# Kernel optimization log

Hardware: AMD Instinct MI355X
Metric: run time of the kernel (lower is better)

The kernel has to match this reference:

```python
import jax, jax.numpy as jnp
import numpy as np

B, S, HID, NH = 2, 2048, 2048, 16
HD = HID // NH          # head_size = 128
ROPE_THETA = 10000.0
SCALING = HD ** -0.5


def setup_inputs() -> dict:
    key = jax.random.key(0)
    ks = jax.random.split(key, 8)
    std = 1.0 / np.sqrt(HID)
    inp = {
        "hidden_states": jax.random.normal(ks[0], (B, S, HID), jnp.float32),
        "positions": jnp.broadcast_to(jnp.arange(S, dtype=jnp.int32), (B, S)),
        "wq": jax.random.normal(ks[1], (HID, HID), jnp.float32) * std,
        "bq": jax.random.normal(ks[2], (HID,), jnp.float32) * 0.02,
        "wk": jax.random.normal(ks[3], (HID, HID), jnp.float32) * std,
        "bk": jax.random.normal(ks[4], (HID,), jnp.float32) * 0.02,
        "wv": jax.random.normal(ks[5], (HID, HID), jnp.float32) * std,
        "bv": jax.random.normal(ks[6], (HID,), jnp.float32) * 0.02,
        "wc": jax.random.normal(ks[7], (HID, HID), jnp.float32) * std,
    }
    return inp


def _rope_neox(x, positions):
    # x: [B, S, NH, HD]; positions: [B, S] int
    half = HD // 2
    inv_freq = 1.0 / (ROPE_THETA ** (jnp.arange(half, dtype=jnp.float32) * (2.0 / HD)))
    freqs = positions.astype(jnp.float32)[..., None] * inv_freq      # [B,S,half]
    cos = jnp.cos(freqs)[:, :, None, :]                               # [B,S,1,half]
    sin = jnp.sin(freqs)[:, :, None, :]
    x1, x2 = x[..., :half], x[..., half:]
    return jnp.concatenate([x1 * cos - x2 * sin, x2 * cos + x1 * sin], axis=-1)


def reference(hidden_states, positions, wq, bq, wk, bk, wv, bv, wc):
    # fused QKV projections
    q = hidden_states @ wq + bq
    k = hidden_states @ wk + bk
    v = hidden_states @ wv + bv
    q = q.reshape(B, S, NH, HD)
    k = k.reshape(B, S, NH, HD)
    v = v.reshape(B, S, NH, HD)
    # neox-style rotary embedding over full head dim
    q = _rope_neox(q, positions)
    k = _rope_neox(k, positions)
    # causal self-attention (prefill path of RadixAttention)
    scores = jnp.einsum("bqhd,bkhd->bhqk", q, k) * SCALING
    causal = jnp.tril(jnp.ones((S, S), dtype=bool))
    scores = jnp.where(causal, scores, jnp.finfo(scores.dtype).min)
    probs = jax.nn.softmax(scores, axis=-1)
    attn = jnp.einsum("bhqk,bkhd->bqhd", probs, v).reshape(B, S, HID)
    # output projection (no bias)
    return attn @ wc
```

## Files before the change

kernel.cpp:

```cpp
#include <hip/hip_runtime.h>
#include <stdint.h>

constexpr int Bsz = 2;
constexpr int Ssz = 2048;
constexpr int Hid = 2048;
constexpr int NHd = 16;
constexpr int Hd  = 128;
constexpr int Mrows = Bsz * Ssz;
constexpr float kScale = 0.08838834764831845f;

typedef __bf16 bf16;
typedef __bf16 bf16x8 __attribute__((ext_vector_type(8)));
typedef __bf16 bf16x4 __attribute__((ext_vector_type(4)));
typedef float  f32x4  __attribute__((ext_vector_type(4)));
typedef float  f32x16 __attribute__((ext_vector_type(16)));

__device__ __forceinline__ void gload_lds16(const bf16* g, bf16* l) {
  __builtin_amdgcn_global_load_lds((const __attribute__((address_space(1))) void*)g,
                                   (__attribute__((address_space(3))) void*)l, 16, 0, 0);
}

__device__ __forceinline__ uint32_t pkbf(bf16 a, bf16 b) {
  union { bf16 hh[2]; uint32_t u; } x;
  x.hh[0] = a; x.hh[1] = b;
  return x.u;
}
__device__ __forceinline__ uint32_t pkff(float a, float b) {
  return pkbf((bf16)a, (bf16)b);
}

__global__ void k_cvt(const float* __restrict__ in, bf16* __restrict__ out, int n4) {
  int i = blockIdx.x * blockDim.x + threadIdx.x;
  if (i >= n4) return;
  float4 v = ((const float4*)in)[i];
  bf16x4 o = { (bf16)v.x, (bf16)v.y, (bf16)v.z, (bf16)v.w };
  ((bf16x4*)out)[i] = o;
}

__global__ void k_wtrans(const float* __restrict__ w0, const float* __restrict__ w1,
                         const float* __restrict__ w2, const float* __restrict__ w3,
                         bf16* __restrict__ out) {
  __shared__ float tile[32][33];
  int z = blockIdx.z;
  const float* w = (z == 0) ? w0 : (z == 1) ? w1 : (z == 2) ? w2 : w3;
  bf16* o = out + (size_t)z * Hid * Hid;
  int n0 = blockIdx.x * 32, k0 = blockIdx.y * 32;
  int tx = threadIdx.x, ty = threadIdx.y;
#pragma unroll
  for (int i = 0; i < 4; i++)
    tile[ty + i * 8][tx] = w[(size_t)(k0 + ty + i * 8) * Hid + n0 + tx];
  __syncthreads();
#pragma unroll
  for (int i = 0; i < 4; i++)
    o[(size_t)(n0 + ty + i * 8) * Hid + k0 + tx] = (bf16)tile[tx][ty + i * 8];
}

__device__ __forceinline__ bf16x8 rdfrag(const bf16* t, int row, int kslot) {
  return *(const bf16x8*)((const char*)t + row * 128 + (((kslot ^ (row & 7)) & 7) << 4));
}

template <int NB>
__device__ __forceinline__ void stageN(const bf16* g, bf16* l, int w, int lane) {
  const int rsub = lane >> 3;
  const int slot = (lane & 7) ^ rsub;
#pragma unroll
  for (int j = 0; j < NB; ++j) {
    const int blk = w * NB + j;
    gload_lds16(g + (size_t)(blk * 8 + rsub) * Hid + slot * 8, l + blk * 512);
  }
}

#define PH_SYNC()                                      \
  __builtin_amdgcn_s_barrier();                        \
  asm volatile("s_waitcnt lgkmcnt(0)" ::: "memory");   \
  __builtin_amdgcn_sched_barrier(0);

template <int MODE>
__global__ __launch_bounds__(512, 2) void k_gemm(const bf16* __restrict__ A,
                                                 const bf16* __restrict__ Bt,
                                                 const float* __restrict__ biasq,
                                                 const float* __restrict__ biask,
                                                 const float* __restrict__ biasv,
                                                 bf16* __restrict__ Qo, bf16* __restrict__ Ko,
                                                 bf16* __restrict__ Vo, float* __restrict__ Fo) {
  constexpr int KK = Hid;
  constexpr int NT = KK / 64;
  __shared__ bf16 smA[2][256 * 64];
  __shared__ bf16 smB[2][128 * 64];
  const int nwg = gridDim.x * gridDim.y;
  int flat = blockIdx.y * gridDim.x + blockIdx.x;
  flat = (flat & 7) * (nwg >> 3) + (flat >> 3);
  const int m0 = (flat / gridDim.x) * 256;
  const int n0 = (flat % gridDim.x) * 128;
  const int tid = threadIdx.x, lane = tid & 63, w = tid >> 6;
  const int wm = w >> 1, wn = w & 1;
  const int frow = lane & 15, a4 = lane >> 4;
  const bf16* Ag = A + (size_t)m0 * KK;
  const bf16* Bg = Bt + (size_t)n0 * KK;
  f32x4 acc[4][4] = {};
  stageN<4>(Ag, smA[0], w, lane);
  stageN<2>(Bg, smB[0], w, lane);
  __syncthreads();
#pragma unroll 2
  for (int kt = 0; kt < NT; ++kt) {
    const int cur = kt & 1;
    const bf16* At = smA[cur];
    const bf16* Btl = smB[cur];
    bf16* As2 = smA[cur ^ 1];
    bf16* Bs2 = smB[cur ^ 1];
    const int kn = (kt + 1 < NT ? kt + 1 : kt) * 64;
    bf16x8 af[2][2], bfr[4][2];
#pragma unroll
    for (int mi = 0; mi < 2; ++mi)
#pragma unroll
      for (int kk = 0; kk < 2; ++kk)
        af[mi][kk] = rdfrag(At, wm * 64 + mi * 16 + frow, kk * 4 + a4);
#pragma unroll
    for (int ni = 0; ni < 4; ++ni)
#pragma unroll
      for (int kk = 0; kk < 2; ++kk)
        bfr[ni][kk] = rdfrag(Btl, wn * 64 + ni * 16 + frow, kk * 4 + a4);
    stageN<4>(Ag + kn, As2, w, lane);
    PH_SYNC();
    __builtin_amdgcn_s_setprio(1);
#pragma unroll
    for (int mi = 0; mi < 2; ++mi)
#pragma unroll
      for (int ni = 0; ni < 4; ++ni)
#pragma unroll
        for (int kk = 0; kk < 2; ++kk)
          acc[mi][ni] = __builtin_amdgcn_mfma_f32_16x16x32_bf16(
              af[mi][kk], bfr[ni][kk], acc[mi][ni], 0, 0, 0);
    __builtin_amdgcn_s_setprio(0);
    __builtin_amdgcn_s_barrier();
#pragma unroll
    for (int mi = 0; mi < 2; ++mi)
#pragma unroll
      for (int kk = 0; kk < 2; ++kk)
        af[mi][kk] = rdfrag(At, wm * 64 + (2 + mi) * 16 + frow, kk * 4 + a4);
    stageN<2>(Bg + kn, Bs2, w, lane);
    PH_SYNC();
    __builtin_amdgcn_s_setprio(1);
#pragma unroll
    for (int mi = 0; mi < 2; ++mi)
#pragma unroll
      for (int ni = 0; ni < 4; ++ni)
#pragma unroll
        for (int kk = 0; kk < 2; ++kk)
          acc[2 + mi][ni] = __builtin_amdgcn_mfma_f32_16x16x32_bf16(
              af[mi][kk], bfr[ni][kk], acc[2 + mi][ni], 0, 0, 0);
    __builtin_amdgcn_s_setprio(0);
    asm volatile("s_waitcnt vmcnt(0)" ::: "memory");
    __builtin_amdgcn_s_barrier();
  }
  if (MODE == 0) {
    const int z = n0 >> 11;
    const float* bias = (z == 0) ? biasq : (z == 1) ? biask : biasv;
    bf16* o = (z == 0) ? Qo : (z == 1) ? Ko : Vo;
    const float oscale = (z == 1) ? (float)(0.08838834764831845 * 1.4426950408889634) : 1.0f;
#pragma unroll
    for (int ni = 0; ni < 4; ++ni) {
      const int col = n0 + wn * 64 + ni * 16 + frow;
      const float bb_ = bias[col & 2047];
      const int h = (col >> 7) & 15, hd = col & (Hd - 1);
#pragma unroll
      for (int mi = 0; mi < 4; ++mi) {
#pragma unroll
        for (int r = 0; r < 4; ++r) {
          const int row = m0 + wm * 64 + mi * 16 + a4 * 4 + r;
          const int bb = row >> 11, ss = row & (Ssz - 1);
          o[(((size_t)bb * NHd + h) * Ssz + ss) * Hd + hd] = (bf16)((acc[mi][ni][r] + bb_) * oscale);
        }
      }
    }
  } else {
#pragma unroll
    for (int mi = 0; mi < 4; ++mi)
#pragma unroll
      for (int ni = 0; ni < 4; ++ni) {
        const int col = n0 + wn * 64 + ni * 16 + frow;
#pragma unroll
        for (int r = 0; r < 4; ++r) {
          const int row = m0 + wm * 64 + mi * 16 + a4 * 4 + r;
          Fo[(size_t)row * Hid + col] = acc[mi][ni][r];
        }
      }
  }
}

__global__ void k_rope(bf16* __restrict__ Q, bf16* __restrict__ Kk, const int* __restrict__ pos) {
  const int idx = blockIdx.x * 256 + threadIdx.x;
  const int i = idx & 63;
  const int s = (idx >> 6) & (Ssz - 1);
  const int bh = idx >> 17;
  const int b = bh >> 4;
  const float p = (float)pos[b * Ssz + s];
  const float f = p * exp2f(-(float)i * 0.20762050593046014f);
  float sn, cs;
  sincosf(f, &sn, &cs);
  const size_t base = ((size_t)bh * Ssz + s) * Hd;
  float x1 = (float)Q[base + i], x2 = (float)Q[base + i + 64];
  Q[base + i]      = (bf16)(x1 * cs - x2 * sn);
  Q[base + i + 64] = (bf16)(x2 * cs + x1 * sn);
  x1 = (float)Kk[base + i]; x2 = (float)Kk[base + i + 64];
  Kk[base + i]      = (bf16)(x1 * cs - x2 * sn);
  Kk[base + i + 64] = (bf16)(x2 * cs + x1 * sn);
}

__global__ __launch_bounds__(256, 2) void k_attn(const bf16* __restrict__ Qg,
                                                 const bf16* __restrict__ Kg,
                                                 const bf16* __restrict__ Vg,
                                                 bf16* __restrict__ AO) {
  const int bh = blockIdx.y;
  int qc = blockIdx.x;
  if (bh & 1) qc = 15 - qc;
  const int tid = threadIdx.x, lane = tid & 63, w = tid >> 6;
  const int l31 = lane & 31, h = lane >> 5;
  __shared__ bf16 Ks[64 * 128];
  __shared__ bf16 Vt[128 * 72];
  const size_t hbase = (size_t)bh * Ssz * Hd;
  const int q0 = qc * 128 + w * 32;
  bf16x8 qf[8];
  {
    const bf16* qp = Qg + hbase + (size_t)(q0 + l31) * Hd + h * 8;
#pragma unroll
    for (int c = 0; c < 8; c++) qf[c] = *(const bf16x8*)(qp + c * 16);
  }
  float m = -1e30f, lsum = 0.f;
  f32x16 o[4] = {};
  const int NT = 2 * (qc + 1);
  for (int t = 0; t < NT; ++t) {
    const int kv0 = t * 64;
    __syncthreads();
    {
      const bf16* Kt = Kg + hbase + (size_t)kv0 * Hd;
#pragma unroll
      for (int i = 0; i < 4; i++) {
        const int db  = (w * 4 + i) * 1024 + (lane << 4);
        const int row = db >> 8;
        const int cb  = (db & 255) ^ ((row & 7) << 4);
        gload_lds16(Kt + row * Hd + (cb >> 1), Ks + (w * 4 + i) * 512);
      }
    }
    {
      const int r4  = (tid >> 4) << 2;
      const int hd0 = (tid & 15) << 3;
      bf16x8 vv[4];
#pragma unroll
      for (int p = 0; p < 4; p++)
        vv[p] = *(const bf16x8*)(Vg + hbase + (size_t)(kv0 + r4 + p) * Hd + hd0);
#pragma unroll
      for (int j = 0; j < 8; j++) {
        uint2 wv;
        wv.x = pkbf(vv[0][j], vv[1][j]);
        wv.y = pkbf(vv[2][j], vv[3][j]);
        const int hd = hd0 + j;
        const int cb = (r4 * 2) ^ (((hd >> 3) & 7) << 4);
        *(uint2*)((char*)Vt + hd * 144 + cb) = wv;
      }
    }
    __syncthreads();
    if (kv0 <= q0 + 31) {
      f32x16 s0 = {}, s1 = {};
#pragma unroll
      for (int c = 0; c < 8; c++) {
        const int cb = (c * 32 + h * 16) ^ ((l31 & 7) << 4);
        bf16x8 k0 = *(const bf16x8*)((const char*)Ks + l31 * 256 + cb);
        bf16x8 k1 = *(const bf16x8*)((const char*)Ks + (32 + l31) * 256 + cb);
        s0 = __builtin_amdgcn_mfma_f32_32x32x16_bf16(k0, qf[c], s0, 0, 0, 0);
        s1 = __builtin_amdgcn_mfma_f32_32x32x16_bf16(k1, qf[c], s1, 0, 0, 0);
      }
      if (kv0 + 63 > q0) {
        const int qg = q0 + l31;
        const int kb = kv0 + 4 * h;
#pragma unroll
        for (int r = 0; r < 16; r++) {
          const int cr = (r & 3) + 8 * (r >> 2);
          if (kb + cr > qg)      s0[r] = -1e30f;
          if (kb + 32 + cr > qg) s1[r] = -1e30f;
        }
      }
      float tm = s0[0];
#pragma unroll
      for (int r = 1; r < 16; r++) tm = fmaxf(tm, s0[r]);
#pragma unroll
      for (int r = 0; r < 16; r++) tm = fmaxf(tm, s1[r]);
      tm = fmaxf(tm, __shfl_xor(tm, 32));
      if (!__all(tm - m <= 8.0f)) {
        const float mn = fmaxf(m, tm);
        const float rs = exp2f(m - mn);
        m = mn; lsum *= rs;
#pragma unroll
        for (int ct = 0; ct < 4; ct++)
#pragma unroll
          for (int r = 0; r < 16; r++) o[ct][r] *= rs;
      }
      float ps = 0.f;
#pragma unroll
      for (int r = 0; r < 16; r++) { s0[r] = exp2f(s0[r] - m); ps += s0[r]; }
#pragma unroll
      for (int r = 0; r < 16; r++) { s1[r] = exp2f(s1[r] - m); ps += s1[r]; }
      ps += __shfl_xor(ps, 32);
      lsum += ps;
      uint32_t gw[8][2];
#pragma unroll
      for (int g = 0; g < 4; g++) {
        gw[g][0]     = pkff(s0[4 * g], s0[4 * g + 1]);
        gw[g][1]     = pkff(s0[4 * g + 2], s0[4 * g + 3]);
        gw[4 + g][0] = pkff(s1[4 * g], s1[4 * g + 1]);
        gw[4 + g][1] = pkff(s1[4 * g + 2], s1[4 * g + 3]);
      }
#pragma unroll
      for (int kc = 0; kc < 4; kc++) {
        const uint32_t a0 = gw[2 * kc][0], a1 = gw[2 * kc][1];
        const uint32_t b0 = gw[2 * kc + 1][0], b1 = gw[2 * kc + 1][1];
        const uint32_t sd0 = h ? a0 : b0, sd1 = h ? a1 : b1;
        const uint32_t r0 = (uint32_t)__shfl_xor((int)sd0, 32);
        const uint32_t r1 = (uint32_t)__shfl_xor((int)sd1, 32);
        union { uint32_t u[4]; bf16x8 v; } pa;
        pa.u[0] = h ? r0 : a0; pa.u[1] = h ? r1 : a1;
        pa.u[2] = h ? b0 : r0; pa.u[3] = h ? b1 : r1;
#pragma unroll
        for (int ct = 0; ct < 4; ct++) {
          const int row = ct * 32 + l31;
          const int cb = (kc * 32 + h * 16) ^ (((row >> 3) & 7) << 4);
          bf16x8 vf = *(const bf16x8*)((const char*)Vt + row * 144 + cb);
          o[ct] = __builtin_amdgcn_mfma_f32_32x32x16_bf16(pa.v, vf, o[ct], 0, 0, 0);
        }
      }
    }
  }
  const float linv = 1.0f / lsum;
  float li[16];
#pragma unroll
  for (int r = 0; r < 16; r++)
    li[r] = __shfl(linv, (r & 3) + 8 * (r >> 2) + 4 * h);
  const int b = bh >> 4, hh = bh & 15;
#pragma unroll
  for (int ct = 0; ct < 4; ct++) {
#pragma unroll
    for (int r = 0; r < 16; r++) {
      const int qrow = q0 + (r & 3) + 8 * (r >> 2) + 4 * h;
      AO[((size_t)b * Ssz + qrow) * Hid + hh * Hd + ct * 32 + l31] = (bf16)(o[ct][r] * li[r]);
    }
  }
}

extern "C" void kernel_launch(void* const* d_in, const int* in_sizes, int n_in,
                              void* d_out, int out_size, void* d_ws, size_t ws_size,
                              hipStream_t stream) {
  (void)in_sizes; (void)n_in; (void)out_size; (void)ws_size;
  const float* hidden   = (const float*)d_in[0];
  const int*   positions= (const int*)d_in[1];
  const float* wq = (const float*)d_in[2];
  const float* bq = (const float*)d_in[3];
  const float* wk = (const float*)d_in[4];
  const float* bk = (const float*)d_in[5];
  const float* wv = (const float*)d_in[6];
  const float* bv = (const float*)d_in[7];
  const float* wc = (const float*)d_in[8];
  float* out = (float*)d_out;

  char* ws = (char*)d_ws;
  bf16* WT  = (bf16*)ws;
  bf16* Hbf = (bf16*)(ws + (size_t)4 * Hid * Hid * 2);
  bf16* Qb  = (bf16*)(ws + (size_t)4 * Hid * Hid * 2 + (size_t)Mrows * Hid * 2);
  bf16* Kb  = Qb + (size_t)Mrows * Hid;
  bf16* Vb  = Kb + (size_t)Mrows * Hid;

  k_cvt<<<dim3(Mrows * Hid / 4 / 256), dim3(256), 0, stream>>>(hidden, Hbf, Mrows * Hid / 4);
  k_wtrans<<<dim3(Hid / 32, Hid / 32, 4), dim3(32, 8), 0, stream>>>(wq, wk, wv, wc, WT);
  k_gemm<0><<<dim3(48, 16), dim3(512), 0, stream>>>(
      Hbf, WT, bq, bk, bv, Qb, Kb, Vb, nullptr);
  k_rope<<<dim3(Bsz * NHd * Ssz * 64 / 256), dim3(256), 0, stream>>>(Qb, Kb, positions);
  k_attn<<<dim3(16, Bsz * NHd), dim3(256), 0, stream>>>(Qb, Kb, Vb, Hbf );
  k_gemm<1><<<dim3(16, 16), dim3(512), 0, stream>>>(
      Hbf, WT + (size_t)3 * Hid * Hid, nullptr, nullptr, nullptr,
      nullptr, nullptr, nullptr, out);
}
```

Before: 301.2 us.

## Triple-buffer GEMM loads, chunked tile swizzle, and double-buffer attention K/V

The GEMM moves from double to triple buffering of its LDS tiles and prefetches two k-steps ahead with partial vmcnt waits. Its block remapping now walks chunked tiles (CHM x CHN per XCD chunk) to improve L2 reuse. The attention kernel double-buffers K and V in LDS and prefetches the next tile's K/V while the current one is computed. The larger LDS footprint lowers GEMM occupancy to one block per CU (launch bounds 512,1), and the new waitcnt counts must exactly match the number of outstanding loads.

```diff
diff --git a/kernel.cpp b/kernel.cpp
--- a/kernel.cpp
+++ b/kernel.cpp
@@ -7,7 +7,6 @@
 constexpr int NHd = 16;
 constexpr int Hd  = 128;
 constexpr int Mrows = Bsz * Ssz;
-constexpr float kScale = 0.08838834764831845f;
 
 typedef __bf16 bf16;
 typedef __bf16 bf16x8 __attribute__((ext_vector_type(8)));
@@ -75,8 +74,8 @@
   asm volatile("s_waitcnt lgkmcnt(0)" ::: "memory");   \
   __builtin_amdgcn_sched_barrier(0);
 
-template <int MODE>
-__global__ __launch_bounds__(512, 2) void k_gemm(const bf16* __restrict__ A,
+template <int MODE, int CHM, int CHN>
+__global__ __launch_bounds__(512, 1) void k_gemm(const bf16* __restrict__ A,
                                                  const bf16* __restrict__ Bt,
                                                  const float* __restrict__ biasq,
                                                  const float* __restrict__ biask,
@@ -85,13 +84,15 @@
                                                  bf16* __restrict__ Vo, float* __restrict__ Fo) {
   constexpr int KK = Hid;
   constexpr int NT = KK / 64;
-  __shared__ bf16 smA[2][256 * 64];
-  __shared__ bf16 smB[2][128 * 64];
-  const int nwg = gridDim.x * gridDim.y;
-  int flat = blockIdx.y * gridDim.x + blockIdx.x;
-  flat = (flat & 7) * (nwg >> 3) + (flat >> 3);
-  const int m0 = (flat / gridDim.x) * 256;
-  const int n0 = (flat % gridDim.x) * 128;
+  __shared__ bf16 smA[3][256 * 64];
+  __shared__ bf16 smB[3][128 * 64];
+  const int hw = blockIdx.y * gridDim.x + blockIdx.x;
+  const int chunk = hw & 7, within = hw >> 3;
+  const int chunk_rows = gridDim.y / CHM;
+  const int cr = chunk % chunk_rows, cc = chunk / chunk_rows;
+  const int mt = cr * CHM + within % CHM;
+  const int nt = cc * CHN + within / CHM;
+  const int m0 = mt * 256, n0 = nt * 128;
   const int tid = threadIdx.x, lane = tid & 63, w = tid >> 6;
   const int wm = w >> 1, wn = w & 1;
   const int frow = lane & 15, a4 = lane >> 4;
@@ -100,15 +101,16 @@
   f32x4 acc[4][4] = {};
   stageN<4>(Ag, smA[0], w, lane);
   stageN<2>(Bg, smB[0], w, lane);
-  __syncthreads();
-#pragma unroll 2
+  stageN<4>(Ag + 64, smA[1], w, lane);
+  stageN<2>(Bg + 64, smB[1], w, lane);
+  asm volatile("s_waitcnt vmcnt(6)" ::: "memory");
+  __builtin_amdgcn_s_barrier();
   for (int kt = 0; kt < NT; ++kt) {
-    const int cur = kt & 1;
-    const bf16* At = smA[cur];
-    const bf16* Btl = smB[cur];
-    bf16* As2 = smA[cur ^ 1];
-    bf16* Bs2 = smB[cur ^ 1];
-    const int kn = (kt + 1 < NT ? kt + 1 : kt) * 64;
+    const bf16* At  = smA[kt % 3];
+    const bf16* Btl = smB[kt % 3];
+    bf16* As2 = smA[(kt + 2) % 3];
+    bf16* Bs2 = smB[(kt + 2) % 3];
+    const int kn2 = (kt + 2 < NT ? kt + 2 : kt) * 64;
     bf16x8 af[2][2], bfr[4][2];
 #pragma unroll
     for (int mi = 0; mi < 2; ++mi)
@@ -120,7 +122,7 @@
 #pragma unroll
       for (int kk = 0; kk < 2; ++kk)
         bfr[ni][kk] = rdfrag(Btl, wn * 64 + ni * 16 + frow, kk * 4 + a4);
-    stageN<4>(Ag + kn, As2, w, lane);
+    stageN<4>(Ag + kn2, As2, w, lane);
     PH_SYNC();
     __builtin_amdgcn_s_setprio(1);
 #pragma unroll
@@ -138,7 +140,7 @@
 #pragma unroll
       for (int kk = 0; kk < 2; ++kk)
         af[mi][kk] = rdfrag(At, wm * 64 + (2 + mi) * 16 + frow, kk * 4 + a4);
-    stageN<2>(Bg + kn, Bs2, w, lane);
+    stageN<2>(Bg + kn2, Bs2, w, lane);
     PH_SYNC();
     __builtin_amdgcn_s_setprio(1);
 #pragma unroll
@@ -150,7 +152,8 @@
           acc[2 + mi][ni] = __builtin_amdgcn_mfma_f32_16x16x32_bf16(
               af[mi][kk], bfr[ni][kk], acc[2 + mi][ni], 0, 0, 0);
     __builtin_amdgcn_s_setprio(0);
-    asm volatile("s_waitcnt vmcnt(0)" ::: "memory");
+    asm volatile("s_waitcnt vmcnt(6)" ::: "memory");
+    __builtin_amdgcn_sched_barrier(0);
     __builtin_amdgcn_s_barrier();
   }
   if (MODE == 0) {
@@ -216,8 +219,8 @@
   if (bh & 1) qc = 15 - qc;
   const int tid = threadIdx.x, lane = tid & 63, w = tid >> 6;
   const int l31 = lane & 31, h = lane >> 5;
-  __shared__ bf16 Ks[64 * 128];
-  __shared__ bf16 Vt[128 * 72];
+  __shared__ bf16 Ks[2][64 * 128];
+  __shared__ bf16 Vt[2][128 * 72];
   const size_t hbase = (size_t)bh * Ssz * Hd;
   const int q0 = qc * 128 + w * 32;
   bf16x8 qf[8];
@@ -229,44 +232,58 @@
   float m = -1e30f, lsum = 0.f;
   f32x16 o[4] = {};
   const int NT = 2 * (qc + 1);
+  const int r4  = (tid >> 4) << 2;
+  const int hd0 = (tid & 15) << 3;
+  bf16x8 vv[4];
+#pragma unroll
+  for (int p = 0; p < 4; p++)
+    vv[p] = *(const bf16x8*)(Vg + hbase + (size_t)(r4 + p) * Hd + hd0);
+  __builtin_amdgcn_sched_barrier(0);
+#pragma unroll
+  for (int i = 0; i < 4; i++) {
+    const int db  = (w * 4 + i) * 1024 + (lane << 4);
+    const int row = db >> 8;
+    const int cb  = (db & 255) ^ ((row & 7) << 4);
+    gload_lds16(Kg + hbase + row * Hd + (cb >> 1), Ks[0] + (w * 4 + i) * 512);
+  }
   for (int t = 0; t < NT; ++t) {
     const int kv0 = t * 64;
-    __syncthreads();
-    {
-      const bf16* Kt = Kg + hbase + (size_t)kv0 * Hd;
-#pragma unroll
-      for (int i = 0; i < 4; i++) {
-        const int db  = (w * 4 + i) * 1024 + (lane << 4);
-        const int row = db >> 8;
-        const int cb  = (db & 255) ^ ((row & 7) << 4);
-        gload_lds16(Kt + row * Hd + (cb >> 1), Ks + (w * 4 + i) * 512);
-      }
-    }
-    {
-      const int r4  = (tid >> 4) << 2;
-      const int hd0 = (tid & 15) << 3;
-      bf16x8 vv[4];
-#pragma unroll
-      for (int p = 0; p < 4; p++)
-        vv[p] = *(const bf16x8*)(Vg + hbase + (size_t)(kv0 + r4 + p) * Hd + hd0);
-#pragma unroll
-      for (int j = 0; j < 8; j++) {
-        uint2 wv;
-        wv.x = pkbf(vv[0][j], vv[1][j]);
-        wv.y = pkbf(vv[2][j], vv[3][j]);
-        const int hd = hd0 + j;
-        const int cb = (r4 * 2) ^ (((hd >> 3) & 7) << 4);
-        *(uint2*)((char*)Vt + hd * 144 + cb) = wv;
-      }
-    }
-    __syncthreads();
+    const int cur = t & 1;
+    asm volatile("s_waitcnt vmcnt(4)" ::: "memory");
+#pragma unroll
+    for (int j = 0; j < 8; j++) {
+      uint2 wv;
+      wv.x = pkbf(vv[0][j], vv[1][j]);
+      wv.y = pkbf(vv[2][j], vv[3][j]);
+      const int hd = hd0 + j;
+      const int cb = (r4 * 2) ^ (((hd >> 3) & 7) << 4);
+      *(uint2*)((char*)(Vt[cur]) + hd * 144 + cb) = wv;
+    }
+    const int tn = (t + 1 < NT) ? t + 1 : t;
+    const size_t nb = (size_t)tn * 64;
+#pragma unroll
+    for (int p = 0; p < 4; p++)
+      vv[p] = *(const bf16x8*)(Vg + hbase + (nb + r4 + p) * Hd + hd0);
+    __builtin_amdgcn_sched_barrier(0);
+#pragma unroll
+    for (int i = 0; i < 4; i++) {
+      const int db  = (w * 4 + i) * 1024 + (lane << 4);
+      const int row = db >> 8;
+      const int cb  = (db & 255) ^ ((row & 7) << 4);
+      gload_lds16(Kg + hbase + (nb + row) * Hd + (cb >> 1), Ks[cur ^ 1] + (w * 4 + i) * 512);
+    }
+    asm volatile("s_waitcnt vmcnt(8) lgkmcnt(0)" ::: "memory");
+    __builtin_amdgcn_sched_barrier(0);
+    __builtin_amdgcn_s_barrier();
     if (kv0 <= q0 + 31) {
+      const bf16* KsC = Ks[cur];
+      const bf16* VtC = Vt[cur];
       f32x16 s0 = {}, s1 = {};
 #pragma unroll
       for (int c = 0; c < 8; c++) {
         const int cb = (c * 32 + h * 16) ^ ((l31 & 7) << 4);
-        bf16x8 k0 = *(const bf16x8*)((const char*)Ks + l31 * 256 + cb);
-        bf16x8 k1 = *(const bf16x8*)((const char*)Ks + (32 + l31) * 256 + cb);
+        bf16x8 k0 = *(const bf16x8*)((const char*)KsC + l31 * 256 + cb);
+        bf16x8 k1 = *(const bf16x8*)((const char*)KsC + (32 + l31) * 256 + cb);
         s0 = __builtin_amdgcn_mfma_f32_32x32x16_bf16(k0, qf[c], s0, 0, 0, 0);
         s1 = __builtin_amdgcn_mfma_f32_32x32x16_bf16(k1, qf[c], s1, 0, 0, 0);
       }
@@ -324,11 +341,12 @@
         for (int ct = 0; ct < 4; ct++) {
           const int row = ct * 32 + l31;
           const int cb = (kc * 32 + h * 16) ^ (((row >> 3) & 7) << 4);
-          bf16x8 vf = *(const bf16x8*)((const char*)Vt + row * 144 + cb);
+          bf16x8 vf = *(const bf16x8*)((const char*)VtC + row * 144 + cb);
           o[ct] = __builtin_amdgcn_mfma_f32_32x32x16_bf16(pa.v, vf, o[ct], 0, 0, 0);
         }
       }
     }
+    __builtin_amdgcn_s_barrier();
   }
   const float linv = 1.0f / lsum;
   float li[16];
@@ -370,11 +388,11 @@
 
   k_cvt<<<dim3(Mrows * Hid / 4 / 256), dim3(256), 0, stream>>>(hidden, Hbf, Mrows * Hid / 4);
   k_wtrans<<<dim3(Hid / 32, Hid / 32, 4), dim3(32, 8), 0, stream>>>(wq, wk, wv, wc, WT);
-  k_gemm<0><<<dim3(48, 16), dim3(512), 0, stream>>>(
+  k_gemm<0, 8, 12><<<dim3(48, 16), dim3(512), 0, stream>>>(
       Hbf, WT, bq, bk, bv, Qb, Kb, Vb, nullptr);
   k_rope<<<dim3(Bsz * NHd * Ssz * 64 / 256), dim3(256), 0, stream>>>(Qb, Kb, positions);
   k_attn<<<dim3(16, Bsz * NHd), dim3(256), 0, stream>>>(Qb, Kb, Vb, Hbf );
-  k_gemm<1><<<dim3(16, 16), dim3(512), 0, stream>>>(
+  k_gemm<1, 4, 8><<<dim3(16, 16), dim3(512), 0, stream>>>(
       Hbf, WT + (size_t)3 * Hid * Hid, nullptr, nullptr, nullptr,
       nullptr, nullptr, nullptr, out);
 }
```

After: 293.5 us. 1.03x faster.
